# Kernel optimization log

Hardware: AMD Instinct MI355X
Metric: run time of the kernel (lower is better)

## Reference

```python
import jax, jax.numpy as jnp
import numpy as np

TOP_K = 2          # routed top_k = top_k - num_shared_experts = 3 - 1
CAP_FACTOR = 1.1   # capacity_factor


def setup_inputs() -> dict:
    key = jax.random.key(0)
    ks = jax.random.split(key, 12)
    B, S, D, E = 4, 2048, 1024, 7
    s = 0.02
    return {
        "x": jax.random.normal(ks[0], (B, S, D), jnp.float32),
        "noise": jax.random.normal(ks[1], (B, S, E), jnp.float32),
        "Wr": jax.random.normal(ks[2], (D, E)) * s, "br": jnp.zeros((E,)),
        "Wn": jax.random.normal(ks[3], (D, E)) * s, "bn": jnp.zeros((E,)),
        "W1": jax.random.normal(ks[4], (E, D, D)) * s, "b1": jnp.zeros((E, D)),
        "W2": jax.random.normal(ks[5], (E, D, D)) * s, "b2": jnp.zeros((E, D)),
        "Ws1": jax.random.normal(ks[6], (D, D)) * s, "bs1": jnp.zeros((D,)),
        "Ws2": jax.random.normal(ks[7], (D, D)) * s, "bs2": jnp.zeros((D,)),
    }


def reference(x, noise, Wr, br, Wn, bn, W1, b1, W2, b2, Ws1, bs1, Ws2, bs2):
    B, S, D = x.shape
    E = Wr.shape[1]
    N = B * S
    C = int(N * TOP_K / E * CAP_FACTOR)  # per-expert capacity (static)

    # shared expert (Dropout inactive at inference)
    x_shared = jax.nn.relu(x @ Ws1 + bs1) @ Ws2 + bs2

    # --- noisy top-k router ---
    logits = x @ Wr + br
    noisy = logits + noise * jax.nn.softplus(x @ Wn + bn)
    vals, idx = jax.lax.top_k(noisy, TOP_K)                    # [B,S,K]
    onehot = jax.nn.one_hot(idx, E, dtype=x.dtype)             # [B,S,K,E]
    probs_k = jax.nn.softmax(vals, axis=-1)                    # softmax over -inf-masked logits == softmax over top-k vals
    router_probs = jnp.einsum('bske,bsk->bse', onehot, probs_k)
    expert_mask = onehot.sum(-2)
    lbl = E * (router_probs.mean((0, 1)) * expert_mask.mean((0, 1))).sum()

    # --- capacity-limited dispatch, first-come-first-served in flat token order ---
    flat_x = x.reshape(N, D)
    flat_g = router_probs.reshape(N, E)
    m = (expert_mask.reshape(N, E) > 0).T                      # [E,N] token->expert assignment
    pos = jnp.cumsum(m.astype(jnp.int32), axis=1) - 1          # slot within expert
    valid = m & (pos < C)
    token = jnp.arange(N, dtype=jnp.int32)
    dest = jnp.where(valid, jnp.arange(E, dtype=jnp.int32)[:, None] * C + pos, E * C)
    idxs = jnp.full((E * C + 1,), N, dtype=jnp.int32)
    idxs = idxs.at[dest.reshape(-1)].set(jnp.broadcast_to(token, (E, N)).reshape(-1))
    idxs = idxs[:E * C].reshape(E, C)                          # token id per slot, N = padding

    xpad = jnp.concatenate([flat_x, jnp.zeros((1, D), x.dtype)], axis=0)
    gpad = jnp.concatenate([flat_g, jnp.zeros((1, E), x.dtype)], axis=0)
    xe = xpad[idxs]                                            # [E,C,D]
    h = jax.nn.relu(jnp.einsum('ecd,edh->ech', xe, W1) + b1[:, None, :])
    out = jnp.einsum('ech,ehd->ecd', h, W2) + b2[:, None, :]
    g = (gpad[idxs] * jnp.eye(E, dtype=x.dtype)[:, None, :]).sum(-1)  # [E,C] gate per slot
    slot_valid = (idxs < N).astype(x.dtype)
    weighted = out * (g * slot_valid)[..., None]

    upd = jnp.zeros((N + 1, D), x.dtype).at[idxs.reshape(-1)].add(weighted.reshape(-1, D))[:N]
    final = upd.reshape(B, S, D) + x_shared
    return final, lbl
```

## Files before the change

### kernel.cpp

```cpp
#include <hip/hip_runtime.h>
#include <math.h>

typedef unsigned short u16;
typedef __attribute__((ext_vector_type(4))) float f32x4;
typedef __bf16 bf16x8 __attribute__((ext_vector_type(8)));

#define NTOK 8192
#define DDIM 1024
#define NEXP 7
#define CAPC 2574
#define CPAD 2688
#define EBLK 1176
#define TBLK 1688
#define XCHK 211

__device__ inline float bf2f(u16 u) {
    union { unsigned int i; float f; } c; c.i = ((unsigned int)u) << 16; return c.f;
}
__device__ inline u16 f2bf(float f) {
    union { float f; unsigned int i; } c; c.f = f;
    unsigned int u = c.i;
    unsigned int r = (u + 0x7fffu + ((u >> 16) & 1u)) >> 16;
    return (u16)r;
}

__device__ inline void gl2lds16(const u16* g, const u16* l) {
    __builtin_amdgcn_global_load_lds(
        (const __attribute__((address_space(1))) unsigned int*)g,
        (__attribute__((address_space(3))) unsigned int*)l, 16, 0, 0);
}

__global__ void k_zero(float* out, long n) {
    long i = (long)blockIdx.x * 256 + threadIdx.x;
    long stride = (long)gridDim.x * 256;
    for (; i < n; i += stride) out[i] = 0.f;
}

__device__ inline void tile_transpose(const float* __restrict__ src, u16* __restrict__ dst,
                                      int k0, int n0, int tid, u16 (*tbuf)[256]) {
#pragma unroll
    for (int p = 0; p < 16; ++p) {
        int kl = p * 16 + (tid >> 4);
        int nl = (tid & 15) * 4;
        float4 v = *(const float4*)(src + (long)(k0 + kl) * 1024 + n0 + nl);
        int s = (tid & 7) << 3;
        int kx = kl ^ s;
        tbuf[nl + 0][kx] = f2bf(v.x);
        tbuf[nl + 1][kx] = f2bf(v.y);
        tbuf[nl + 2][kx] = f2bf(v.z);
        tbuf[nl + 3][kx] = f2bf(v.w);
    }
    __syncthreads();
#pragma unroll
    for (int q = 0; q < 8; ++q) {
        int nl = q * 8 + (tid >> 5);
        int kl = (tid & 31) * 8;
        int s = ((nl >> 2) & 7) << 3;
        const u16* pr = &tbuf[nl][kl ^ s];
        ushort4 a = *(const ushort4*)pr;
        ushort4 b = *(const ushort4*)(pr + 4);
        u16* pd = dst + (long)(n0 + nl) * 1024 + k0 + kl;
        *(ushort4*)pd = a;
        *(ushort4*)(pd + 4) = b;
    }
}

__global__ void k_prep(int* __restrict__ slot_token, u16* __restrict__ zrow,
                       const float* __restrict__ W1, const float* __restrict__ Ws1,
                       u16* __restrict__ Wt, u16* __restrict__ Wst,
                       const float* __restrict__ W2, const float* __restrict__ Ws2,
                       u16* __restrict__ Wt2, u16* __restrict__ Wst2, int ntb) {
    __shared__ u16 tbuf[64][256];
    int bid = blockIdx.x, tid = threadIdx.x;
    if (bid >= ntb) {
        int gid = (bid - ntb) * 256 + tid;
        if (gid < NEXP * CPAD) slot_token[gid] = NTOK;
        if (gid < DDIM) zrow[gid] = 0;
        return;
    }
    int set = bid >> 9;
    int t9 = bid & 511;
    int z = t9 >> 6;
    int rem = t9 & 63;
    int k0 = (rem >> 4) * 256;
    int n0 = (rem & 15) * 64;
    const float* srcE = set ? W2 : W1;
    const float* srcS = set ? Ws2 : Ws1;
    u16* dE = set ? Wt2 : Wt;
    u16* dS = set ? Wst2 : Wst;
    const float* src; u16* dst;
    if (z < 7) { src = srcE + (long)z * 1048576; dst = dE + (long)z * 1048576; }
    else       { src = srcS;                     dst = dS; }
    tile_transpose(src, dst, k0, n0, tid, tbuf);
}

__global__ void k_transpose(const float* __restrict__ srcE, const float* __restrict__ srcS,
                            u16* __restrict__ Wt, u16* __restrict__ Wst) {
    __shared__ u16 tbuf[64][256];
    int bid = blockIdx.x, tid = threadIdx.x;
    int z = bid >> 6;
    int rem = bid & 63;
    int k0 = (rem >> 4) * 256;
    int n0 = (rem & 15) * 64;
    const float* src; u16* dst;
    if (z < 7) { src = srcE + (long)z * 1048576; dst = Wt + (long)z * 1048576; }
    else       { src = srcS;                     dst = Wst; }
    tile_transpose(src, dst, k0, n0, tid, tbuf);
}

__global__ __launch_bounds__(512) void k_router(
    const float* __restrict__ x,
    const float* __restrict__ Wr, const float* __restrict__ Wn,
    const float* __restrict__ br, const float* __restrict__ bn,
    const float* __restrict__ noise,
    u16* __restrict__ xb,
    int* __restrict__ idx0, int* __restrict__ idx1,
    float* __restrict__ p0, float* __restrict__ p1,
    int* __restrict__ cnt8, double* __restrict__ sum8) {
    __shared__ float swr[7][1024];
    __shared__ float swn[7][1024];
    __shared__ int sb0[8], sb1[8];
    __shared__ double sq0[8], sq1[8];
    int tid = threadIdx.x;
    for (int i = tid; i < 7168; i += 512) {
        int d = i / 7, e = i - d * 7;
        float vr = Wr[i], vn = Wn[i];
        swr[e][d] = vr; swn[e][d] = vn;
    }
    __syncthreads();
    int lane = tid & 63, wv = tid >> 6;
    int t = blockIdx.x * 8 + wv;
    double ar[7] = {0,0,0,0,0,0,0}, an[7] = {0,0,0,0,0,0,0};
#pragma unroll
    for (int j = 0; j < 4; ++j) {
        int d0 = j * 256 + lane * 4;
        float4 xv = *(const float4*)(x + (long)t * 1024 + d0);
        ushort4 o; o.x = f2bf(xv.x); o.y = f2bf(xv.y); o.z = f2bf(xv.z); o.w = f2bf(xv.w);
        *(ushort4*)(xb + (long)t * 1024 + d0) = o;
#pragma unroll
        for (int e = 0; e < 7; ++e) {
            float4 w4 = *(const float4*)&swr[e][d0];
            float4 n4 = *(const float4*)&swn[e][d0];
            ar[e] += (double)xv.x * (double)w4.x; an[e] += (double)xv.x * (double)n4.x;
            ar[e] += (double)xv.y * (double)w4.y; an[e] += (double)xv.y * (double)n4.y;
            ar[e] += (double)xv.z * (double)w4.z; an[e] += (double)xv.z * (double)n4.z;
            ar[e] += (double)xv.w * (double)w4.w; an[e] += (double)xv.w * (double)n4.w;
        }
    }
#pragma unroll
    for (int e = 0; e < 7; ++e) {
        for (int o = 32; o > 0; o >>= 1) {
            ar[e] += __shfl_xor(ar[e], o);
            an[e] += __shfl_xor(an[e], o);
        }
    }
    if (lane == 0) {
        double best = -1e300, second = -1e300; int b0 = 0, b1 = 0;
#pragma unroll
        for (int e = 0; e < 7; ++e) {
            double lg = ar[e] + (double)br[e];
            double z  = an[e] + (double)bn[e];
            double sp = (z > 30.0) ? (z + log1p(exp(-z))) : log1p(exp(z));
            double v  = lg + (double)noise[t * 7 + e] * sp;
            if (v > best)        { second = best; b1 = b0; best = v; b0 = e; }
            else if (v > second) { second = v; b1 = e; }
        }
        double ex = exp(second - best);
        double q0 = 1.0 / (1.0 + ex);
        double q1 = ex / (1.0 + ex);
        idx0[t] = b0; idx1[t] = b1; p0[t] = (float)q0; p1[t] = (float)q1;
        sb0[wv] = b0; sb1[wv] = b1; sq0[wv] = q0; sq1[wv] = q1;
    }
    __syncthreads();
    if (tid < 7) {
        int c = 0; double s = 0.0;
#pragma unroll
        for (int w = 0; w < 8; ++w) {
            if (sb0[w] == tid) { c++; s += sq0[w]; }
            if (sb1[w] == tid) { c++; s += sq1[w]; }
        }
        cnt8[tid * 1024 + blockIdx.x] = c;
        sum8[tid * 1024 + blockIdx.x] = s;
    }
}

__global__ void k_scanbase(const int* __restrict__ cnt8, const double* __restrict__ sum8,
                           int* __restrict__ base8, int* __restrict__ cnt,
                           float* __restrict__ out) {
    __shared__ int s[7][128];
    __shared__ double rd[7][128];
    __shared__ int rawc[7];
    __shared__ double ps[7];
    int tid = threadIdx.x;
    int e = tid >> 7, i = tid & 127;
    int c8[8]; int v = 0; double s64 = 0.0;
#pragma unroll
    for (int j = 0; j < 8; ++j) {
        c8[j] = cnt8[e * 1024 + i * 8 + j];
        v += c8[j];
        s64 += sum8[e * 1024 + i * 8 + j];
    }
    s[e][i] = v;
    rd[e][i] = s64;
    __syncthreads();
    for (int o = 1; o < 128; o <<= 1) {
        int add = (i >= o) ? s[e][i - o] : 0;
        __syncthreads();
        s[e][i] += add;
        __syncthreads();
    }
    int run = s[e][i] - v;
#pragma unroll
    for (int j = 0; j < 8; ++j) { base8[e * 1024 + i * 8 + j] = run; run += c8[j]; }
    if (i == 127) { rawc[e] = s[e][127]; cnt[e] = (s[e][127] < CAPC) ? s[e][127] : CAPC; }
    for (int o = 64; o > 0; o >>= 1) {
        if (i < o) rd[e][i] += rd[e][i + o];
        __syncthreads();
    }
    if (i == 0) ps[e] = rd[e][0];
    __syncthreads();
    if (tid == 0) {
        double acc = 0.0;
        for (int ee = 0; ee < 7; ++ee) acc += ps[ee] * (double)rawc[ee];
        out[(long)NTOK * DDIM] = (float)(7.0 * acc / (8192.0 * 8192.0));
    }
}

__global__ void k_assign(const int* __restrict__ idx0, const int* __restrict__ idx1,
                         const int* __restrict__ base8, int* __restrict__ slot_token,
                         int* __restrict__ ts0, int* __restrict__ ts1) {
    int t = blockIdx.x * 256 + threadIdx.x;
    int lane = threadIdx.x & 63;
    int i0 = idx0[t], i1 = idx1[t];
    int myts0 = -1, myts1 = -1;
    unsigned long long gm = 0xFFull << ((lane >> 3) * 8);
    unsigned long long lt = (1ull << lane) - 1ull;
    int chunk = t >> 3;
#pragma unroll
    for (int e = 0; e < 7; ++e) {
        bool has = (i0 == e) || (i1 == e);
        unsigned long long m = __ballot(has);
        int pre = __popcll(m & lt & gm);
        int pos = base8[e * 1024 + chunk] + pre;
        if (has && pos < CAPC) {
            int slot = e * CPAD + pos;
            slot_token[slot] = t;
            if (i0 == e) myts0 = slot; else myts1 = slot;
        }
    }
    ts0[t] = myts0; ts1[t] = myts1;
}

template <bool GATHER, bool MODE_H>
__global__ __launch_bounds__(256) void k_gemm(
    const u16* __restrict__ AbaseE, const u16* __restrict__ AbaseS,
    const int* __restrict__ gidx, const u16* __restrict__ zrow,
    const u16* __restrict__ WtE, const u16* __restrict__ WtS,
    const float* __restrict__ biasE, const float* __restrict__ biasS,
    u16* __restrict__ outE, u16* __restrict__ outS,
    const int* __restrict__ cnt) {
    __shared__ __align__(16) u16 ldsA[128 * 64];
    __shared__ __align__(16) u16 ldsB[128 * 64];
    int phys = blockIdx.x;
    int bid = (phys & 7) * XCHK + (phys >> 3);
    int tid = threadIdx.x, lane = tid & 63, wv = tid >> 6;
    int lrow = lane >> 3, lkg = lane & 7;
    int kgs = lkg ^ lrow;

    int e = 0, my, nx;
    const u16* Ab; const u16* Bb; const float* bias; u16* outp;
    bool gather = false;
    if (bid < EBLK) {
        e = bid / 168; int r = bid % 168; my = r >> 3; nx = r & 7;
        if (my * 128 >= cnt[e]) return;
        Ab = AbaseE + (GATHER ? 0L : (long)e * CPAD * 1024);
        Bb = WtE + ((long)e << 20);
        bias = biasE + e * 1024;
        outp = outE + (long)e * CPAD * 1024;
        gather = GATHER;
    } else {
        int sb = bid - EBLK; my = sb >> 3; nx = sb & 7;
        Ab = AbaseS; Bb = WtS; bias = biasS; outp = outS;
    }
    int m0 = my * 128, n0 = nx * 128;

    const u16* arow[4];
    const u16* brow[4];
#pragma unroll
    for (int i = 0; i < 4; ++i) {
        int r = (wv * 4 + i) * 8 + lrow;
        if (gather) {
            int tok = gidx[e * CPAD + m0 + r];
            arow[i] = (tok < NTOK) ? (AbaseE + (long)tok * DDIM) : zrow;
        } else {
            arow[i] = Ab + (long)(m0 + r) * DDIM;
        }
        brow[i] = Bb + (long)(n0 + r) * DDIM;
    }
    f32x4 acc[4][4];
#pragma unroll
    for (int a = 0; a < 4; ++a)
#pragma unroll
        for (int b = 0; b < 4; ++b) { f32x4 z = {0.f, 0.f, 0.f, 0.f}; acc[a][b] = z; }

    int wm = (wv >> 1) * 64, wn = (wv & 1) * 64;
    int rl = lane & 15, quad = lane >> 4;

    for (int k0 = 0; k0 < 1024; k0 += 64) {
#pragma unroll
        for (int i = 0; i < 4; ++i) {
            gl2lds16(arow[i] + k0 + kgs * 8, &ldsA[(wv * 4 + i) * 512]);
            gl2lds16(brow[i] + k0 + kgs * 8, &ldsB[(wv * 4 + i) * 512]);
        }
        __syncthreads();
#pragma unroll
        for (int ks = 0; ks < 2; ++ks) {
            int kg = ks * 4 + quad;
            bf16x8 af[4], bf[4];
#pragma unroll
            for (int mi = 0; mi < 4; ++mi) {
                int row = wm + mi * 16 + rl;
                af[mi] = *(const bf16x8*)&ldsA[row * 64 + (kg ^ (row & 7)) * 8];
            }
#pragma unroll
            for (int ni = 0; ni < 4; ++ni) {
                int row = wn + ni * 16 + rl;
                bf[ni] = *(const bf16x8*)&ldsB[row * 64 + (kg ^ (row & 7)) * 8];
            }
#pragma unroll
            for (int mi = 0; mi < 4; ++mi)
#pragma unroll
                for (int ni = 0; ni < 4; ++ni)
                    acc[mi][ni] = __builtin_amdgcn_mfma_f32_16x16x32_bf16(
                        af[mi], bf[ni], acc[mi][ni], 0, 0, 0);
        }
        __syncthreads();
    }
#pragma unroll
    for (int ni = 0; ni < 4; ++ni) {
        int col = n0 + wn + ni * 16 + rl;
        float bv = bias[col];
#pragma unroll
        for (int mi = 0; mi < 4; ++mi) {
            int rowb = m0 + wm + mi * 16 + quad * 4;
#pragma unroll
            for (int r = 0; r < 4; ++r) {
                float v = acc[mi][ni][r] + bv;
                if constexpr (MODE_H) v = v > 0.f ? v : 0.f;
                outp[(long)(rowb + r) * DDIM + col] = f2bf(v);
            }
        }
    }
}

__global__ __launch_bounds__(256) void k_combine(
    const u16* __restrict__ Xs, const u16* __restrict__ OutE,
    const int* __restrict__ ts0, const int* __restrict__ ts1,
    const float* __restrict__ p0, const float* __restrict__ p1,
    float* __restrict__ out) {
    int b = blockIdx.x;
    int d = threadIdx.x * 4;
    long base = (long)b * DDIM + d;
    ushort4 xs4 = *(const ushort4*)(Xs + base);
    float r0 = bf2f(xs4.x), r1 = bf2f(xs4.y), r2 = bf2f(xs4.z), r3 = bf2f(xs4.w);
    int s0 = ts0[b], s1 = ts1[b];
    if (s0 >= 0) {
        float g = p0[b];
        ushort4 o4 = *(const ushort4*)(OutE + (long)s0 * DDIM + d);
        r0 += g * bf2f(o4.x); r1 += g * bf2f(o4.y); r2 += g * bf2f(o4.z); r3 += g * bf2f(o4.w);
    }
    if (s1 >= 0) {
        float g = p1[b];
        ushort4 o4 = *(const ushort4*)(OutE + (long)s1 * DDIM + d);
        r0 += g * bf2f(o4.x); r1 += g * bf2f(o4.y); r2 += g * bf2f(o4.z); r3 += g * bf2f(o4.w);
    }
    float4 w; w.x = r0; w.y = r1; w.z = r2; w.w = r3;
    *(float4*)(out + base) = w;
}

extern "C" void kernel_launch(void* const* d_in, const int* in_sizes, int n_in,
                              void* d_out, int out_size, void* d_ws, size_t ws_size,
                              hipStream_t stream) {
    const float* x    = (const float*)d_in[0];
    const float* noise= (const float*)d_in[1];
    const float* Wr   = (const float*)d_in[2];
    const float* br   = (const float*)d_in[3];
    const float* Wn   = (const float*)d_in[4];
    const float* bn   = (const float*)d_in[5];
    const float* W1   = (const float*)d_in[6];
    const float* b1   = (const float*)d_in[7];
    const float* W2   = (const float*)d_in[8];
    const float* b2   = (const float*)d_in[9];
    const float* Ws1  = (const float*)d_in[10];
    const float* bs1  = (const float*)d_in[11];
    const float* Ws2  = (const float*)d_in[12];
    const float* bs2  = (const float*)d_in[13];
    float* out = (float*)d_out;
    char* ws = (char*)d_ws;

    size_t off = 0;
    auto alloc = [&](size_t bytes) { size_t o = off; off += (bytes + 255) & ~(size_t)255; return o; };
    u16*  Wt   = (u16*)(ws + alloc(7ull * 1048576 * 2));
    u16*  Wst  = (u16*)(ws + alloc(1048576ull * 2));
    u16*  xb   = (u16*)(ws + alloc((size_t)NTOK * 1024 * 2));
    u16*  He   = (u16*)(ws + alloc((size_t)NEXP * CPAD * 1024 * 2));
    u16*  Hs   = (u16*)(ws + alloc((size_t)NTOK * 1024 * 2));
    u16*  OutE = (u16*)(ws + alloc((size_t)NEXP * CPAD * 1024 * 2));
    u16*  Xs   = (u16*)(ws + alloc((size_t)NTOK * 1024 * 2));
    int*  idx0 = (int*)(ws + alloc(NTOK * 4));
    int*  idx1 = (int*)(ws + alloc(NTOK * 4));
    float* p0  = (float*)(ws + alloc(NTOK * 4));
    float* p1  = (float*)(ws + alloc(NTOK * 4));
    int*  ts0  = (int*)(ws + alloc(NTOK * 4));
    int*  ts1  = (int*)(ws + alloc(NTOK * 4));
    int*  slot_token = (int*)(ws + alloc(NEXP * CPAD * 4));
    int*  cnt8  = (int*)(ws + alloc(7 * 1024 * 4));
    int*  base8 = (int*)(ws + alloc(7 * 1024 * 4));
    double* sum8 = (double*)(ws + alloc(7 * 1024 * 8));
    int*  cnt    = (int*)(ws + alloc(8 * 4));
    u16*  zrow   = (u16*)(ws + alloc(1024 * 2));
    size_t base_off = off;
    u16*  Wt2  = (u16*)(ws + alloc(7ull * 1048576 * 2));
    u16*  Wst2 = (u16*)(ws + alloc(1048576ull * 2));

    if (base_off > ws_size) {
        k_zero<<<2048, 256, 0, stream>>>(out, (long)out_size);
        return;
    }
    bool sep = (off <= ws_size);
    if (!sep) { Wt2 = Wt; Wst2 = Wst; }
    int ntb = sep ? 1024 : 512;

    k_prep<<<ntb + 74, 256, 0, stream>>>(
        slot_token, zrow, W1, Ws1, Wt, Wst, W2, Ws2, Wt2, Wst2, ntb);
    k_router<<<1024, 512, 0, stream>>>(
        x, Wr, Wn, br, bn, noise, xb, idx0, idx1, p0, p1, cnt8, sum8);
    k_scanbase<<<1, 896, 0, stream>>>(cnt8, sum8, base8, cnt, out);
    k_assign<<<32, 256, 0, stream>>>(idx0, idx1, base8, slot_token, ts0, ts1);

    k_gemm<true, true><<<TBLK, 256, 0, stream>>>(
        xb, xb, slot_token, zrow, Wt, Wst, b1, bs1, He, Hs, cnt);

    if (!sep)
        k_transpose<<<512, 256, 0, stream>>>(W2, Ws2, Wt, Wst);

    k_gemm<false, false><<<TBLK, 256, 0, stream>>>(
        He, Hs, nullptr, zrow, Wt2, Wst2, b2, bs2, OutE, Xs, cnt);

    k_combine<<<NTOK, 256, 0, stream>>>(Xs, OutE, ts0, ts1, p0, p1, out);
    (void)in_sizes; (void)n_in; (void)out_size;
}
```

Baseline: 371.5 us.

## Fuse weight prep into router kernel and merge scan with slot assignment

Weight transpose/convert blocks and slot-table init are folded into the router launch as extra blocks sharing a unioned LDS buffer, so router and weight prep run concurrently in one grid. The single-block scan and the assignment kernel are merged into one 8-block kernel in which each block recomputes the per-expert prefix scan into LDS and then assigns its 1024 tokens, removing the base8 round trip. This cuts launches from four to two but makes every transpose block use 512 threads and the router's large LDS footprint, which may lower occupancy. The scan work is now duplicated across 8 blocks.

```diff
diff --git a/kernel.cpp b/kernel.cpp
--- a/kernel.cpp
+++ b/kernel.cpp
@@ -63,35 +63,6 @@
         *(ushort4*)pd = a;
         *(ushort4*)(pd + 4) = b;
     }
-}
-
-__global__ void k_prep(int* __restrict__ slot_token, u16* __restrict__ zrow,
-                       const float* __restrict__ W1, const float* __restrict__ Ws1,
-                       u16* __restrict__ Wt, u16* __restrict__ Wst,
-                       const float* __restrict__ W2, const float* __restrict__ Ws2,
-                       u16* __restrict__ Wt2, u16* __restrict__ Wst2, int ntb) {
-    __shared__ u16 tbuf[64][256];
-    int bid = blockIdx.x, tid = threadIdx.x;
-    if (bid >= ntb) {
-        int gid = (bid - ntb) * 256 + tid;
-        if (gid < NEXP * CPAD) slot_token[gid] = NTOK;
-        if (gid < DDIM) zrow[gid] = 0;
-        return;
-    }
-    int set = bid >> 9;
-    int t9 = bid & 511;
-    int z = t9 >> 6;
-    int rem = t9 & 63;
-    int k0 = (rem >> 4) * 256;
-    int n0 = (rem & 15) * 64;
-    const float* srcE = set ? W2 : W1;
-    const float* srcS = set ? Ws2 : Ws1;
-    u16* dE = set ? Wt2 : Wt;
-    u16* dS = set ? Wst2 : Wst;
-    const float* src; u16* dst;
-    if (z < 7) { src = srcE + (long)z * 1048576; dst = dE + (long)z * 1048576; }
-    else       { src = srcS;                     dst = dS; }
-    tile_transpose(src, dst, k0, n0, tid, tbuf);
 }
 
 __global__ void k_transpose(const float* __restrict__ srcE, const float* __restrict__ srcS,
@@ -108,7 +79,7 @@
     tile_transpose(src, dst, k0, n0, tid, tbuf);
 }
 
-__global__ __launch_bounds__(512) void k_router(
+__global__ __launch_bounds__(512) void k_front(
     const float* __restrict__ x,
     const float* __restrict__ Wr, const float* __restrict__ Wn,
     const float* __restrict__ br, const float* __restrict__ bn,
@@ -116,20 +87,77 @@
     u16* __restrict__ xb,
     int* __restrict__ idx0, int* __restrict__ idx1,
     float* __restrict__ p0, float* __restrict__ p1,
-    int* __restrict__ cnt8, double* __restrict__ sum8) {
-    __shared__ float swr[7][1024];
-    __shared__ float swn[7][1024];
+    int* __restrict__ cnt8, double* __restrict__ sum8,
+    int* __restrict__ slot_token, u16* __restrict__ zrow,
+    const float* __restrict__ W1, const float* __restrict__ Ws1,
+    u16* __restrict__ Wt, u16* __restrict__ Wst,
+    const float* __restrict__ W2, const float* __restrict__ Ws2,
+    u16* __restrict__ Wt2, u16* __restrict__ Wst2, int ntb) {
+    __shared__ union USM {
+        struct { float swr[7][1024]; float swn[7][1024]; } r;
+        u16 tb[64][256];
+    } sm;
     __shared__ int sb0[8], sb1[8];
     __shared__ double sq0[8], sq1[8];
-    int tid = threadIdx.x;
+    int bid = blockIdx.x, tid = threadIdx.x;
+
+    if (bid >= 1024) {
+        int tbk = bid - 1024;
+        if (tbk >= ntb) {
+            int gid = (tbk - ntb) * 512 + tid;
+            if (gid < NEXP * CPAD) slot_token[gid] = NTOK;
+            if (gid < DDIM) zrow[gid] = 0;
+            return;
+        }
+        int set = tbk >> 9;
+        int t9 = tbk & 511;
+        int z = t9 >> 6;
+        int rem = t9 & 63;
+        int k0 = (rem >> 4) * 256;
+        int n0 = (rem & 15) * 64;
+        const float* srcE = set ? W2 : W1;
+        const float* srcS = set ? Ws2 : Ws1;
+        u16* dE = set ? Wt2 : Wt;
+        u16* dS = set ? Wst2 : Wst;
+        const float* src; u16* dst;
+        if (z < 7) { src = srcE + (long)z * 1048576; dst = dE + (long)z * 1048576; }
+        else       { src = srcS;                     dst = dS; }
+#pragma unroll
+        for (int p = 0; p < 8; ++p) {
+            int kl = p * 32 + (tid >> 4);
+            int nl = (tid & 15) * 4;
+            float4 v = *(const float4*)(src + (long)(k0 + kl) * 1024 + n0 + nl);
+            int s = (tid & 7) << 3;
+            int kx = kl ^ s;
+            sm.tb[nl + 0][kx] = f2bf(v.x);
+            sm.tb[nl + 1][kx] = f2bf(v.y);
+            sm.tb[nl + 2][kx] = f2bf(v.z);
+            sm.tb[nl + 3][kx] = f2bf(v.w);
+        }
+        __syncthreads();
+#pragma unroll
+        for (int q = 0; q < 4; ++q) {
+            int nl = q * 16 + (tid >> 5);
+            int kl = (tid & 31) * 8;
+            int s = ((nl >> 2) & 7) << 3;
+            const u16* pr = &sm.tb[nl][kl ^ s];
+            ushort4 a = *(const ushort4*)pr;
+            ushort4 b = *(const ushort4*)(pr + 4);
+            u16* pd = dst + (long)(n0 + nl) * 1024 + k0 + kl;
+            *(ushort4*)pd = a;
+            *(ushort4*)(pd + 4) = b;
+        }
+        return;
+    }
+
     for (int i = tid; i < 7168; i += 512) {
         int d = i / 7, e = i - d * 7;
-        float vr = Wr[i], vn = Wn[i];
-        swr[e][d] = vr; swn[e][d] = vn;
+        sm.r.swr[e][d] = Wr[i];
+        sm.r.swn[e][d] = Wn[i];
     }
     __syncthreads();
     int lane = tid & 63, wv = tid >> 6;
-    int t = blockIdx.x * 8 + wv;
+    int t = bid * 8 + wv;
     double ar[7] = {0,0,0,0,0,0,0}, an[7] = {0,0,0,0,0,0,0};
 #pragma unroll
     for (int j = 0; j < 4; ++j) {
@@ -139,8 +167,8 @@
         *(ushort4*)(xb + (long)t * 1024 + d0) = o;
 #pragma unroll
         for (int e = 0; e < 7; ++e) {
-            float4 w4 = *(const float4*)&swr[e][d0];
-            float4 n4 = *(const float4*)&swn[e][d0];
+            float4 w4 = *(const float4*)&sm.r.swr[e][d0];
+            float4 n4 = *(const float4*)&sm.r.swn[e][d0];
             ar[e] += (double)xv.x * (double)w4.x; an[e] += (double)xv.x * (double)n4.x;
             ar[e] += (double)xv.y * (double)w4.y; an[e] += (double)xv.y * (double)n4.y;
             ar[e] += (double)xv.z * (double)w4.z; an[e] += (double)xv.z * (double)n4.z;
@@ -179,73 +207,78 @@
             if (sb0[w] == tid) { c++; s += sq0[w]; }
             if (sb1[w] == tid) { c++; s += sq1[w]; }
         }
-        cnt8[tid * 1024 + blockIdx.x] = c;
-        sum8[tid * 1024 + blockIdx.x] = s;
-    }
-}
-
-__global__ void k_scanbase(const int* __restrict__ cnt8, const double* __restrict__ sum8,
-                           int* __restrict__ base8, int* __restrict__ cnt,
-                           float* __restrict__ out) {
+        cnt8[tid * 1024 + bid] = c;
+        sum8[tid * 1024 + bid] = s;
+    }
+}
+
+__global__ __launch_bounds__(1024) void k_scanassign(
+    const int* __restrict__ cnt8, const double* __restrict__ sum8,
+    const int* __restrict__ idx0, const int* __restrict__ idx1,
+    int* __restrict__ slot_token, int* __restrict__ ts0, int* __restrict__ ts1,
+    int* __restrict__ cnt, float* __restrict__ out) {
     __shared__ int s[7][128];
+    __shared__ int b8[7][1024];
     __shared__ double rd[7][128];
     __shared__ int rawc[7];
-    __shared__ double ps[7];
-    int tid = threadIdx.x;
+    int tid = threadIdx.x, bid = blockIdx.x;
     int e = tid >> 7, i = tid & 127;
-    int c8[8]; int v = 0; double s64 = 0.0;
-#pragma unroll
-    for (int j = 0; j < 8; ++j) {
-        c8[j] = cnt8[e * 1024 + i * 8 + j];
-        v += c8[j];
-        s64 += sum8[e * 1024 + i * 8 + j];
-    }
-    s[e][i] = v;
-    rd[e][i] = s64;
+    bool act = (e < 7);
+    int c8[8]; int v = 0;
+    if (act) {
+#pragma unroll
+        for (int j = 0; j < 8; ++j) { c8[j] = cnt8[e * 1024 + i * 8 + j]; v += c8[j]; }
+        s[e][i] = v;
+        if (bid == 0) {
+            double s64 = 0.0;
+#pragma unroll
+            for (int j = 0; j < 8; ++j) s64 += sum8[e * 1024 + i * 8 + j];
+            rd[e][i] = s64;
+        }
+    }
     __syncthreads();
     for (int o = 1; o < 128; o <<= 1) {
-        int add = (i >= o) ? s[e][i - o] : 0;
-        __syncthreads();
-        s[e][i] += add;
-        __syncthreads();
-    }
-    int run = s[e][i] - v;
-#pragma unroll
-    for (int j = 0; j < 8; ++j) { base8[e * 1024 + i * 8 + j] = run; run += c8[j]; }
-    if (i == 127) { rawc[e] = s[e][127]; cnt[e] = (s[e][127] < CAPC) ? s[e][127] : CAPC; }
+        int add = (act && i >= o) ? s[e][i - o] : 0;
+        __syncthreads();
+        if (act) s[e][i] += add;
+        __syncthreads();
+    }
+    if (act) {
+        int run = s[e][i] - v;
+#pragma unroll
+        for (int j = 0; j < 8; ++j) { b8[e][i * 8 + j] = run; run += c8[j]; }
+        if (i == 127) {
+            rawc[e] = s[e][127];
+            if (bid == 0) cnt[e] = (s[e][127] < CAPC) ? s[e][127] : CAPC;
+        }
+    }
     for (int o = 64; o > 0; o >>= 1) {
-        if (i < o) rd[e][i] += rd[e][i + o];
-        __syncthreads();
-    }
-    if (i == 0) ps[e] = rd[e][0];
+        if (bid == 0 && act && i < o) rd[e][i] += rd[e][i + o];
+        __syncthreads();
+    }
+    if (bid == 0 && tid == 0) {
+        double acc = 0.0;
+        for (int ee = 0; ee < 7; ++ee) acc += rd[ee][0] * (double)rawc[ee];
+        out[(long)NTOK * DDIM] = (float)(7.0 * acc / (8192.0 * 8192.0));
+    }
     __syncthreads();
-    if (tid == 0) {
-        double acc = 0.0;
-        for (int ee = 0; ee < 7; ++ee) acc += ps[ee] * (double)rawc[ee];
-        out[(long)NTOK * DDIM] = (float)(7.0 * acc / (8192.0 * 8192.0));
-    }
-}
-
-__global__ void k_assign(const int* __restrict__ idx0, const int* __restrict__ idx1,
-                         const int* __restrict__ base8, int* __restrict__ slot_token,
-                         int* __restrict__ ts0, int* __restrict__ ts1) {
-    int t = blockIdx.x * 256 + threadIdx.x;
-    int lane = threadIdx.x & 63;
+    int t = bid * 1024 + tid;
+    int lane = tid & 63;
     int i0 = idx0[t], i1 = idx1[t];
     int myts0 = -1, myts1 = -1;
     unsigned long long gm = 0xFFull << ((lane >> 3) * 8);
     unsigned long long lt = (1ull << lane) - 1ull;
     int chunk = t >> 3;
 #pragma unroll
-    for (int e = 0; e < 7; ++e) {
-        bool has = (i0 == e) || (i1 == e);
+    for (int ee = 0; ee < 7; ++ee) {
+        bool has = (i0 == ee) || (i1 == ee);
         unsigned long long m = __ballot(has);
         int pre = __popcll(m & lt & gm);
-        int pos = base8[e * 1024 + chunk] + pre;
+        int pos = b8[ee][chunk] + pre;
         if (has && pos < CAPC) {
-            int slot = e * CPAD + pos;
+            int slot = ee * CPAD + pos;
             slot_token[slot] = t;
-            if (i0 == e) myts0 = slot; else myts1 = slot;
+            if (i0 == ee) myts0 = slot; else myts1 = slot;
         }
     }
     ts0[t] = myts0; ts1[t] = myts1;
@@ -415,7 +448,6 @@
     int*  ts1  = (int*)(ws + alloc(NTOK * 4));
     int*  slot_token = (int*)(ws + alloc(NEXP * CPAD * 4));
     int*  cnt8  = (int*)(ws + alloc(7 * 1024 * 4));
-    int*  base8 = (int*)(ws + alloc(7 * 1024 * 4));
     double* sum8 = (double*)(ws + alloc(7 * 1024 * 8));
     int*  cnt    = (int*)(ws + alloc(8 * 4));
     u16*  zrow   = (u16*)(ws + alloc(1024 * 2));
@@ -430,13 +462,14 @@
     bool sep = (off <= ws_size);
     if (!sep) { Wt2 = Wt; Wst2 = Wst; }
     int ntb = sep ? 1024 : 512;
-
-    k_prep<<<ntb + 74, 256, 0, stream>>>(
+    int nib = (NEXP * CPAD + 511) / 512;
+
+    k_front<<<1024 + ntb + nib, 512, 0, stream>>>(
+        x, Wr, Wn, br, bn, noise, xb, idx0, idx1, p0, p1, cnt8, sum8,
         slot_token, zrow, W1, Ws1, Wt, Wst, W2, Ws2, Wt2, Wst2, ntb);
-    k_router<<<1024, 512, 0, stream>>>(
-        x, Wr, Wn, br, bn, noise, xb, idx0, idx1, p0, p1, cnt8, sum8);
-    k_scanbase<<<1, 896, 0, stream>>>(cnt8, sum8, base8, cnt, out);
-    k_assign<<<32, 256, 0, stream>>>(idx0, idx1, base8, slot_token, ts0, ts1);
+
+    k_scanassign<<<8, 1024, 0, stream>>>(
+        cnt8, sum8, idx0, idx1, slot_token, ts0, ts1, cnt, out);
 
     k_gemm<true, true><<<TBLK, 256, 0, stream>>>(
         xb, xb, slot_token, zrow, Wt, Wst, b1, bs1, He, Hs, cnt);
```

After: 375.9 us. No clear change (+1.2%).
